# Performance work log

Measured on AMD Instinct MI355X. Metric: run time of the kernel, lower is better.

The kernel has to match this reference:

```python
import jax, jax.numpy as jnp
import numpy as np

B, TQ, TK, D, H = 2, 2048, 2048, 1024, 16
HD = D // H
MLP = 4 * D
EPS = 1e-5


def _ln(x, g, b):
    m = jnp.mean(x, axis=-1, keepdims=True)
    v = jnp.mean(jnp.square(x - m), axis=-1, keepdims=True)
    return (x - m) * jax.lax.rsqrt(v + EPS) * g + b


def setup_inputs() -> dict:
    key = jax.random.key(0)
    ks = jax.random.split(key, 16)
    s = 0.02
    inp = {
        "x": jax.random.normal(ks[0], (B, TQ, D), jnp.float32),
        "enc_out": jax.random.normal(ks[1], (B, TK, D), jnp.float32),
        "causal_mask": jnp.tril(jnp.ones((TQ, TQ), jnp.int32)),
        # LayerNorm params
        "ln1_g": jnp.ones((D,), jnp.float32), "ln1_b": jnp.zeros((D,), jnp.float32),
        "ln2_g": jnp.ones((D,), jnp.float32), "ln2_b": jnp.zeros((D,), jnp.float32),
        "ln3_g": jnp.ones((D,), jnp.float32), "ln3_b": jnp.zeros((D,), jnp.float32),
        # self-attn (weights stored [in, out])
        "qkv_w": jax.random.normal(ks[2], (D, 3 * D), jnp.float32) * s,
        "qkv_b": jnp.zeros((3 * D,), jnp.float32),
        "proj_w": jax.random.normal(ks[3], (D, D), jnp.float32) * s,
        "proj_b": jnp.zeros((D,), jnp.float32),
        # cross-attn
        "q_w": jax.random.normal(ks[4], (D, D), jnp.float32) * s,
        "q_b": jnp.zeros((D,), jnp.float32),
        "kv_w": jax.random.normal(ks[5], (D, 2 * D), jnp.float32) * s,
        "kv_b": jnp.zeros((2 * D,), jnp.float32),
        "co_w": jax.random.normal(ks[6], (D, D), jnp.float32) * s,
        "co_b": jnp.zeros((D,), jnp.float32),
        # MLP
        "mlp1_w": jax.random.normal(ks[7], (D, MLP), jnp.float32) * s,
        "mlp1_b": jnp.zeros((MLP,), jnp.float32),
        "mlp2_w": jax.random.normal(ks[8], (MLP, D), jnp.float32) * s,
        "mlp2_b": jnp.zeros((D,), jnp.float32),
    }
    return inp


def _self_attn(x, mask, qkv_w, qkv_b, proj_w, proj_b):
    b, t, d = x.shape
    qkv = (x @ qkv_w + qkv_b).reshape(b, t, 3, H, HD)
    q, k, v = qkv[:, :, 0], qkv[:, :, 1], qkv[:, :, 2]  # [b,t,H,HD]
    scale = HD ** (-0.5)
    attn = jnp.einsum('bqhd,bkhd->bhqk', q, k) * scale
    attn = jnp.where(mask[None, None] == 0, -jnp.inf, attn)
    attn = jax.nn.softmax(attn, axis=-1)
    out = jnp.einsum('bhqk,bkhd->bqhd', attn, v).reshape(b, t, d)
    return out @ proj_w + proj_b


def _cross_attn(q_in, kv_in, q_w, q_b, kv_w, kv_b, co_w, co_b):
    b, tq, d = q_in.shape
    tk = kv_in.shape[1]
    Q = (q_in @ q_w + q_b).reshape(b, tq, H, HD)
    KV = (kv_in @ kv_w + kv_b).reshape(b, tk, 2, H, HD)
    K, V = KV[:, :, 0], KV[:, :, 1]
    scale = HD ** (-0.5)
    attn = jnp.einsum('bqhd,bkhd->bhqk', Q, K) * scale
    attn = jax.nn.softmax(attn, axis=-1)
    out = jnp.einsum('bhqk,bkhd->bqhd', attn, V).reshape(b, tq, d)
    return out @ co_w + co_b


def reference(x, enc_out, causal_mask, ln1_g, ln1_b, ln2_g, ln2_b, ln3_g, ln3_b,
              qkv_w, qkv_b, proj_w, proj_b, q_w, q_b, kv_w, kv_b, co_w, co_b,
              mlp1_w, mlp1_b, mlp2_w, mlp2_b):
    x = x + _self_attn(_ln(x, ln1_g, ln1_b), causal_mask, qkv_w, qkv_b, proj_w, proj_b)
    x = x + _cross_attn(_ln(x, ln2_g, ln2_b), enc_out, q_w, q_b, kv_w, kv_b, co_w, co_b)
    h = _ln(x, ln3_g, ln3_b)
    h = jax.nn.gelu(h @ mlp1_w + mlp1_b, approximate=False) @ mlp2_w + mlp2_b
    return x + h
```

## Files before the change

### kernel.cpp

```cpp
#include <hip/hip_runtime.h>
#include <hip/hip_bf16.h>
#include <cstdint>
#include <cstddef>


#define DEV __device__ __forceinline__

typedef short bf16x8 __attribute__((ext_vector_type(8)));
typedef float f32x4  __attribute__((ext_vector_type(4)));

#define QSCALE 0.18033688011112042f

DEV unsigned short f2bf(float f) {
  unsigned int u = __builtin_bit_cast(unsigned int, f);
  u = u + 0x7FFFu + ((u >> 16) & 1u);
  return (unsigned short)(u >> 16);
}

DEV unsigned int cvt_pk_bf16(float lo, float hi) {
  unsigned int r;
  asm volatile("v_cvt_pk_bf16_f32 %0, %1, %2" : "=v"(r) : "v"(lo), "v"(hi));
  return r;
}

DEV void gload_lds16(const void* g, void* lds) {
  __builtin_amdgcn_global_load_lds(
      (const __attribute__((address_space(1))) void*)g,
      (__attribute__((address_space(3))) void*)lds, 16, 0, 0);
}

__global__ __launch_bounds__(256) void k_transpose_bf16(
    const float* __restrict__ in, unsigned short* __restrict__ out, int K, int N,
    int s0, int s1, float sc) {
  __shared__ float tile[32][33];
  const int n0 = blockIdx.x * 32, k0 = blockIdx.y * 32;
  const int tx = threadIdx.x, ty = threadIdx.y;
#pragma unroll
  for (int i = 0; i < 32; i += 8)
    tile[ty + i][tx] = in[(size_t)(k0 + ty + i) * N + n0 + tx];
  __syncthreads();
#pragma unroll
  for (int i = 0; i < 32; i += 8) {
    const int n = n0 + ty + i;
    float v = tile[tx][ty + i];
    if (n >= s0 && n < s1) v *= sc;
    out[(size_t)n * K + k0 + tx] = f2bf(v);
  }
}

__global__ __launch_bounds__(256) void k_scale_bias(
    const float* __restrict__ in, float* __restrict__ out, int n, int s0, int s1, float sc) {
  const int i = blockIdx.x * 256 + threadIdx.x;
  if (i < n) out[i] = in[i] * ((i >= s0 && i < s1) ? sc : 1.0f);
}

__global__ __launch_bounds__(256) void k_vtrans(
    const unsigned short* __restrict__ V, int ldv, int vo0,
    unsigned short* __restrict__ vt, int TK) {
  __shared__ unsigned short tile[32][33];
  const int k0 = blockIdx.x * 32;
  const int d0 = (blockIdx.y & 1) * 32;
  const int bh = blockIdx.z;
  const int b = bh >> 4, h = bh & 15;
  const int tx = threadIdx.x, ty = threadIdx.y;
  const size_t tok0 = (size_t)b * 2048;
#pragma unroll
  for (int i = 0; i < 32; i += 8)
    tile[ty + i][tx] = V[(tok0 + k0 + ty + i) * ldv + vo0 + h * 64 + d0 + tx];
  __syncthreads();
#pragma unroll
  for (int i = 0; i < 32; i += 8)
    vt[((size_t)bh * 64 + d0 + ty + i) * TK + k0 + tx] = tile[tx][ty + i];
}

__global__ __launch_bounds__(256) void k_f32_to_bf16(
    const float* __restrict__ in, unsigned short* __restrict__ out, int n4) {
  const int i = blockIdx.x * 256 + threadIdx.x;
  if (i < n4) {
    const float4 v = ((const float4*)in)[i];
    ushort4 o;
    o.x = f2bf(v.x); o.y = f2bf(v.y); o.z = f2bf(v.z); o.w = f2bf(v.w);
    ((ushort4*)out)[i] = o;
  }
}

__global__ __launch_bounds__(256) void k_ln(
    const float* __restrict__ x, const float* __restrict__ g,
    const float* __restrict__ bt, unsigned short* __restrict__ y) {
  const int row = blockIdx.x, t = threadIdx.x;
  const float4 v = ((const float4*)(x + (size_t)row * 1024))[t];
  float s1 = v.x + v.y + v.z + v.w;
  float s2 = v.x * v.x + v.y * v.y + v.z * v.z + v.w * v.w;
#pragma unroll
  for (int off = 1; off < 64; off <<= 1) {
    s1 += __shfl_xor(s1, off);
    s2 += __shfl_xor(s2, off);
  }
  __shared__ float r1[4], r2[4];
  if ((t & 63) == 0) { r1[t >> 6] = s1; r2[t >> 6] = s2; }
  __syncthreads();
  const float tot1 = r1[0] + r1[1] + r1[2] + r1[3];
  const float tot2 = r2[0] + r2[1] + r2[2] + r2[3];
  const float mean = tot1 * (1.0f / 1024.0f);
  const float var  = tot2 * (1.0f / 1024.0f) - mean * mean;
  const float rstd = rsqrtf(var + 1e-5f);
  const float4 gg = ((const float4*)g)[t];
  const float4 bb = ((const float4*)bt)[t];
  ushort4 o;
  o.x = f2bf((v.x - mean) * rstd * gg.x + bb.x);
  o.y = f2bf((v.y - mean) * rstd * gg.y + bb.y);
  o.z = f2bf((v.z - mean) * rstd * gg.z + bb.z);
  o.w = f2bf((v.w - mean) * rstd * gg.w + bb.w);
  ((ushort4*)(y + (size_t)row * 1024))[t] = o;
}

template <int EPI, int BN>
__global__ __launch_bounds__(256) void k_gemm(
    const unsigned short* __restrict__ A, const unsigned short* __restrict__ Bt,
    const float* __restrict__ bias, const float* __restrict__ resid,
    unsigned short* __restrict__ Obf, float* __restrict__ Of, int N, int K) {
  constexpr int NFR = BN / 32;
  __shared__ __align__(16) unsigned short As[128 * 32];
  __shared__ __align__(16) unsigned short Bs[BN * 32];
  const int tid = threadIdx.x;
  const int wave = tid >> 6, lane = tid & 63;
  const int nwg = gridDim.x * gridDim.y;
  const int wg = blockIdx.y * gridDim.x + blockIdx.x;
  const int swz = (wg & 7) * (nwg >> 3) + (wg >> 3);
  const int bn = swz % gridDim.x, bm = swz / gridDim.x;
  const int la = lane & 15, ks = (lane >> 4) * 8;
  const int wr = wave >> 1, wc = wave & 1;
  f32x4 acc[4][NFR] = {};
  const int rsub = lane >> 2;
  const int kk = (lane & 3) * 8;
  const unsigned short* ga = A  + (size_t)(bm * 128 + wave * 32 + rsub) * K + kk;
  const unsigned short* gb = Bt + (size_t)(bn * BN + wave * (BN / 4) + rsub) * K + kk;
  unsigned short* lA0 = &As[(wave * 32) * 32];
  unsigned short* lA1 = &As[(wave * 32 + 16) * 32];
  unsigned short* lB0 = &Bs[(wave * (BN / 4)) * 32];
  unsigned short* lB1 = &Bs[(wave * (BN / 4) + 16) * 32];
  for (int kt = 0; kt < K; kt += 32) {
    gload_lds16(ga + kt,                  lA0);
    gload_lds16(ga + kt + (size_t)16 * K, lA1);
    gload_lds16(gb + kt,                  lB0);
    if constexpr (BN == 128) gload_lds16(gb + kt + (size_t)16 * K, lB1);
    __syncthreads();
    bf16x8 af[4], bfr[NFR];
#pragma unroll
    for (int m = 0; m < 4; ++m)
      af[m] = *(const bf16x8*)&As[(wr * 64 + m * 16 + la) * 32 + ks];
#pragma unroll
    for (int n = 0; n < NFR; ++n)
      bfr[n] = *(const bf16x8*)&Bs[(wc * (BN / 2) + n * 16 + la) * 32 + ks];
#pragma unroll
    for (int m = 0; m < 4; ++m)
#pragma unroll
      for (int n = 0; n < NFR; ++n)
        acc[m][n] = __builtin_amdgcn_mfma_f32_16x16x32_bf16(af[m], bfr[n], acc[m][n], 0, 0, 0);
    __syncthreads();
  }
#pragma unroll
  for (int m = 0; m < 4; ++m) {
    const int row = bm * 128 + wr * 64 + m * 16 + (lane >> 4) * 4;
#pragma unroll
    for (int n = 0; n < NFR; ++n) {
      const int col = bn * BN + wc * (BN / 2) + n * 16 + la;
      const float bv = bias[col];
#pragma unroll
      for (int r = 0; r < 4; ++r) {
        float v = acc[m][n][r] + bv;
        const size_t idx = (size_t)(row + r) * N + col;
        if constexpr (EPI == 0) {
          Obf[idx] = f2bf(v);
        } else if constexpr (EPI == 1) {
          Of[idx] = v + resid[idx];
        } else {
          v = 0.5f * v * (1.0f + erff(v * 0.70710678118654752f));
          Obf[idx] = f2bf(v);
        }
      }
    }
  }
}

template <bool CAUSAL>
__global__ __launch_bounds__(256) void k_attn4(
    const unsigned short* __restrict__ Qb, int ldq, int qo0,
    const unsigned short* __restrict__ Kb, int ldk, int ko0,
    const unsigned short* __restrict__ Vtg,
    unsigned short* __restrict__ O, int TK) {
  __shared__ __align__(16) unsigned short Ks[2][64 * 64];
  __shared__ __align__(16) unsigned short Vs[2][64 * 64];
  __shared__ __align__(16) unsigned short Pl[4][16 * 64];
  const int qt = (blockIdx.x + blockIdx.y) & 31;
  const int h = blockIdx.y, b = blockIdx.z;
  const int bh = b * 16 + h;
  const int tid = threadIdx.x, wave = tid >> 6, lane = tid & 63;
  const int la = lane & 15, g = lane >> 4;
  const int qoff = qo0 + h * 64, koff = ko0 + h * 64;
  const size_t tok0 = (size_t)b * 2048;

  bf16x8 qf[2];
  {
    const unsigned short* qp =
        Qb + (tok0 + qt * 64 + wave * 16 + la) * ldq + qoff + g * 8;
    qf[0] = *(const bf16x8*)qp;
    qf[1] = *(const bf16x8*)(qp + 32);
  }
  f32x4 oacc[4] = {};
  float m_r = -1e30f, l_r = 0.0f;

  const int nkt = CAUSAL ? (qt + 1) : (TK >> 6);

  const int rr = lane >> 3, cc = lane & 7;
  const int sc = (cc ^ rr) * 8;
  const unsigned short* Vrow = Vtg + (size_t)bh * 64 * TK;
  auto stage = [&](int kt, int buf) {
#pragma unroll
    for (int r = 0; r < 2; ++r) {
      const int row = wave * 8 + r * 32 + rr;
      gload_lds16(Kb + (tok0 + kt * 64 + row) * ldk + koff + sc,
                  &Ks[buf][(wave * 8 + r * 32) * 64]);
      gload_lds16(Vrow + (size_t)row * TK + kt * 64 + sc,
                  &Vs[buf][(wave * 8 + r * 32) * 64]);
    }
  };

  stage(0, 0);
  int cur = 0;
  char* pw = (char*)Pl[wave];
  const int lsw = (la & 7) << 4;

  for (int kt = 0; kt < nkt; ++kt) {
    if (kt + 1 < nkt) {
      stage(kt + 1, cur ^ 1);
      asm volatile("s_waitcnt vmcnt(4)" ::: "memory");
    } else {
      asm volatile("s_waitcnt vmcnt(0)" ::: "memory");
    }
    __builtin_amdgcn_s_barrier();

    f32x4 s[4] = {};
    __builtin_amdgcn_s_setprio(1);
#pragma unroll
    for (int kc = 0; kc < 2; ++kc)
#pragma unroll
      for (int n = 0; n < 4; ++n) {
        const int key = n * 16 + la;
        const bf16x8 kfr = *(const bf16x8*)((const char*)&Ks[cur][0] +
            key * 128 + ((kc * 64 + g * 16) ^ ((key & 7) << 4)));
        s[n] = __builtin_amdgcn_mfma_f32_16x16x32_bf16(kfr, qf[kc], s[n], 0, 0, 0);
      }
    __builtin_amdgcn_s_setprio(0);

    if (CAUSAL && kt == nkt - 1) {
      const int qloc = wave * 16 + la;
#pragma unroll
      for (int n = 0; n < 4; ++n)
#pragma unroll
        for (int r = 0; r < 4; ++r)
          if (n * 16 + g * 4 + r > qloc) s[n][r] = -1e30f;
    }
    float t0 = fmaxf(fmaxf(s[0][0], s[0][1]), fmaxf(s[0][2], s[0][3]));
    float t1 = fmaxf(fmaxf(s[1][0], s[1][1]), fmaxf(s[1][2], s[1][3]));
    float t2 = fmaxf(fmaxf(s[2][0], s[2][1]), fmaxf(s[2][2], s[2][3]));
    float t3 = fmaxf(fmaxf(s[3][0], s[3][1]), fmaxf(s[3][2], s[3][3]));
    float tm = fmaxf(fmaxf(t0, t1), fmaxf(t2, t3));
    tm = fmaxf(tm, __shfl_xor(tm, 16, 64));
    tm = fmaxf(tm, __shfl_xor(tm, 32, 64));
    if (!__all(tm <= m_r + 8.0f)) {
      const float mn = fmaxf(m_r, tm);
      const float al = exp2f(m_r - mn);
      m_r = mn;
      l_r *= al;
#pragma unroll
      for (int n4 = 0; n4 < 4; ++n4)
#pragma unroll
        for (int r = 0; r < 4; ++r) oacc[n4][r] *= al;
    }
    float p[4][4];
#pragma unroll
    for (int n = 0; n < 4; ++n)
#pragma unroll
      for (int r = 0; r < 4; ++r) p[n][r] = exp2f(s[n][r] - m_r);
    float rs = ((p[0][0] + p[0][1]) + (p[0][2] + p[0][3]))
             + ((p[1][0] + p[1][1]) + (p[1][2] + p[1][3]))
             + ((p[2][0] + p[2][1]) + (p[2][2] + p[2][3]))
             + ((p[3][0] + p[3][1]) + (p[3][2] + p[3][3]));
    rs += __shfl_xor(rs, 16, 64);
    rs += __shfl_xor(rs, 32, 64);
    l_r += rs;

#pragma unroll
    for (int n = 0; n < 4; ++n)
#pragma unroll
      for (int rp = 0; rp < 2; ++rp) {
        const unsigned int w = cvt_pk_bf16(p[n][2 * rp], p[n][2 * rp + 1]);
        *(unsigned int*)(pw + la * 128 + ((n * 32 + g * 8 + rp * 4) ^ lsw)) = w;
      }
    asm volatile("s_waitcnt lgkmcnt(0)" ::: "memory");
    bf16x8 pb[2];
    pb[0] = *(const bf16x8*)(pw + la * 128 + ((0 * 64 + g * 16) ^ lsw));
    pb[1] = *(const bf16x8*)(pw + la * 128 + ((1 * 64 + g * 16) ^ lsw));

    __builtin_amdgcn_s_setprio(1);
#pragma unroll
    for (int kc = 0; kc < 2; ++kc)
#pragma unroll
      for (int n4 = 0; n4 < 4; ++n4) {
        const int d = n4 * 16 + la;
        const bf16x8 vb = *(const bf16x8*)((const char*)&Vs[cur][0] +
            d * 128 + ((kc * 64 + g * 16) ^ ((d & 7) << 4)));
        oacc[n4] = __builtin_amdgcn_mfma_f32_16x16x32_bf16(vb, pb[kc], oacc[n4], 0, 0, 0);
      }
    __builtin_amdgcn_s_setprio(0);
    asm volatile("s_waitcnt lgkmcnt(0)" ::: "memory");
    __builtin_amdgcn_s_barrier();
    cur ^= 1;
  }

  const float inv = 1.0f / l_r;
#pragma unroll
  for (int n4 = 0; n4 < 4; ++n4)
#pragma unroll
    for (int rp = 0; rp < 2; ++rp) {
      const unsigned int w = cvt_pk_bf16(oacc[n4][2 * rp] * inv, oacc[n4][2 * rp + 1] * inv);
      *(unsigned int*)(pw + la * 128 + ((n4 * 32 + g * 8 + rp * 4) ^ lsw)) = w;
    }
  asm volatile("s_waitcnt lgkmcnt(0)" ::: "memory");
  const int q2 = lane >> 2, c4 = lane & 3;
  const size_t orow = tok0 + qt * 64 + wave * 16 + q2;
#pragma unroll
  for (int h8 = 0; h8 < 2; ++h8) {
    const bf16x8 v = *(const bf16x8*)(pw + q2 * 128 +
        ((c4 * 32 + h8 * 16) ^ ((q2 & 7) << 4)));
    *(bf16x8*)&O[orow * 1024 + h * 64 + c4 * 16 + h8 * 8] = v;
  }
}

constexpr size_t SZ_1K1K  = 1024ull * 1024 * 2;
constexpr size_t OFF_WQKV = 0;                         constexpr size_t SZ_WQKV = 3072ull * 1024 * 2;
constexpr size_t OFF_WPRJ = OFF_WQKV + SZ_WQKV;
constexpr size_t OFF_WQ   = OFF_WPRJ + SZ_1K1K;
constexpr size_t OFF_WKV  = OFF_WQ + SZ_1K1K;          constexpr size_t SZ_WKV = 2048ull * 1024 * 2;
constexpr size_t OFF_WCO  = OFF_WKV + SZ_WKV;
constexpr size_t OFF_WM1  = OFF_WCO + SZ_1K1K;         constexpr size_t SZ_WM1 = 4096ull * 1024 * 2;
constexpr size_t OFF_WM2  = OFF_WM1 + SZ_WM1;          constexpr size_t SZ_WM2 = 1024ull * 4096 * 2;
constexpr size_t OFF_ENCB = OFF_WM2 + SZ_WM2;          constexpr size_t SZ_ACT = 4096ull * 1024 * 2;
constexpr size_t OFF_XCUR = OFF_ENCB + SZ_ACT;         constexpr size_t SZ_XF  = 4096ull * 1024 * 4;
constexpr size_t OFF_LNO  = OFF_XCUR + SZ_XF;
constexpr size_t OFF_BIG  = OFF_LNO + SZ_ACT;          constexpr size_t SZ_BIG = 4096ull * 4096 * 2;
constexpr size_t OFF_ATTN = OFF_BIG + SZ_BIG;
constexpr size_t OFF_QPRJ = OFF_ATTN + SZ_ACT;
constexpr size_t OFF_BQKV = OFF_QPRJ + SZ_ACT;
constexpr size_t OFF_BQ   = OFF_BQKV + 3072 * 4;
constexpr size_t WS_NEED  = OFF_BQ + 1024 * 4;

extern "C" void kernel_launch(void* const* d_in, const int* in_sizes, int n_in,
                              void* d_out, int out_size, void* d_ws, size_t ws_size,
                              hipStream_t stream) {
  (void)in_sizes; (void)n_in; (void)out_size;
  if (ws_size < WS_NEED) return;

  const float* x     = (const float*)d_in[0];
  const float* enc   = (const float*)d_in[1];
  const float* ln1g  = (const float*)d_in[3];
  const float* ln1b  = (const float*)d_in[4];
  const float* ln2g  = (const float*)d_in[5];
  const float* ln2b  = (const float*)d_in[6];
  const float* ln3g  = (const float*)d_in[7];
  const float* ln3b  = (const float*)d_in[8];
  const float* qkv_w = (const float*)d_in[9];
  const float* qkv_b = (const float*)d_in[10];
  const float* prj_w = (const float*)d_in[11];
  const float* prj_b = (const float*)d_in[12];
  const float* q_w   = (const float*)d_in[13];
  const float* q_b   = (const float*)d_in[14];
  const float* kv_w  = (const float*)d_in[15];
  const float* kv_b  = (const float*)d_in[16];
  const float* co_w  = (const float*)d_in[17];
  const float* co_b  = (const float*)d_in[18];
  const float* m1_w  = (const float*)d_in[19];
  const float* m1_b  = (const float*)d_in[20];
  const float* m2_w  = (const float*)d_in[21];
  const float* m2_b  = (const float*)d_in[22];
  float* out = (float*)d_out;

  char* ws = (char*)d_ws;
  unsigned short* wqkv = (unsigned short*)(ws + OFF_WQKV);
  unsigned short* wprj = (unsigned short*)(ws + OFF_WPRJ);
  unsigned short* wq   = (unsigned short*)(ws + OFF_WQ);
  unsigned short* wkv  = (unsigned short*)(ws + OFF_WKV);
  unsigned short* wco  = (unsigned short*)(ws + OFF_WCO);
  unsigned short* wm1  = (unsigned short*)(ws + OFF_WM1);
  unsigned short* wm2  = (unsigned short*)(ws + OFF_WM2);
  unsigned short* encb = (unsigned short*)(ws + OFF_ENCB);
  float*          xcur = (float*)(ws + OFF_XCUR);
  unsigned short* lno  = (unsigned short*)(ws + OFF_LNO);
  unsigned short* big  = (unsigned short*)(ws + OFF_BIG);
  unsigned short* attnb= (unsigned short*)(ws + OFF_ATTN);
  unsigned short* qprj = (unsigned short*)(ws + OFF_QPRJ);
  float*          bqkv = (float*)(ws + OFF_BQKV);
  float*          bq   = (float*)(ws + OFF_BQ);
  unsigned short* vtS  = big + (size_t)4096 * 3072;
  unsigned short* vtC  = big + (size_t)4096 * 2048;

  const dim3 tb(32, 8);
  k_transpose_bf16<<<dim3(3072/32, 1024/32), tb, 0, stream>>>(qkv_w, wqkv, 1024, 3072, 0, 1024, QSCALE);
  k_transpose_bf16<<<dim3(1024/32, 1024/32), tb, 0, stream>>>(prj_w, wprj, 1024, 1024, 0, 0, 1.0f);
  k_transpose_bf16<<<dim3(1024/32, 1024/32), tb, 0, stream>>>(q_w,   wq,   1024, 1024, 0, 1024, QSCALE);
  k_transpose_bf16<<<dim3(2048/32, 1024/32), tb, 0, stream>>>(kv_w,  wkv,  1024, 2048, 0, 0, 1.0f);
  k_transpose_bf16<<<dim3(1024/32, 1024/32), tb, 0, stream>>>(co_w,  wco,  1024, 1024, 0, 0, 1.0f);
  k_transpose_bf16<<<dim3(4096/32, 1024/32), tb, 0, stream>>>(m1_w,  wm1,  1024, 4096, 0, 0, 1.0f);
  k_transpose_bf16<<<dim3(1024/32, 4096/32), tb, 0, stream>>>(m2_w,  wm2,  4096, 1024, 0, 0, 1.0f);
  k_scale_bias<<<12, 256, 0, stream>>>(qkv_b, bqkv, 3072, 0, 1024, QSCALE);
  k_scale_bias<<<4, 256, 0, stream>>>(q_b, bq, 1024, 0, 1024, QSCALE);
  k_f32_to_bf16<<<4096, 256, 0, stream>>>(enc, encb, 1048576);

  k_ln<<<4096, 256, 0, stream>>>(x, ln1g, ln1b, lno);
  k_gemm<0,128><<<dim3(24, 32), 256, 0, stream>>>(lno, wqkv, bqkv, nullptr, big, nullptr, 3072, 1024);
  k_vtrans<<<dim3(64, 2, 32), tb, 0, stream>>>(big, 3072, 2048, vtS, 2048);
  k_attn4<true><<<dim3(32, 16, 2), 256, 0, stream>>>(big, 3072, 0,
                                                     big, 3072, 1024,
                                                     vtS, attnb, 2048);
  k_gemm<1,64><<<dim3(16, 32), 256, 0, stream>>>(attnb, wprj, prj_b, x, nullptr, xcur, 1024, 1024);

  k_ln<<<4096, 256, 0, stream>>>(xcur, ln2g, ln2b, lno);
  k_gemm<0,64><<<dim3(16, 32), 256, 0, stream>>>(lno,  wq,  bq,   nullptr, qprj, nullptr, 1024, 1024);
  k_gemm<0,128><<<dim3(16, 32), 256, 0, stream>>>(encb, wkv, kv_b, nullptr, big,  nullptr, 2048, 1024);
  k_vtrans<<<dim3(64, 2, 32), tb, 0, stream>>>(big, 2048, 1024, vtC, 2048);
  k_attn4<false><<<dim3(32, 16, 2), 256, 0, stream>>>(qprj, 1024, 0,
                                                      big,  2048, 0,
                                                      vtC, attnb, 2048);
  k_gemm<1,64><<<dim3(16, 32), 256, 0, stream>>>(attnb, wco, co_b, xcur, nullptr, xcur, 1024, 1024);

  k_ln<<<4096, 256, 0, stream>>>(xcur, ln3g, ln3b, lno);
  k_gemm<2,128><<<dim3(32, 32), 256, 0, stream>>>(lno, wm1, m1_b, nullptr, big, nullptr, 4096, 1024);
  k_gemm<1,64><<<dim3(16, 32), 256, 0, stream>>>(big, wm2, m2_b, xcur, nullptr, out, 1024, 4096);
}
```

Before: 651.0 us.

## Software-pipeline attention: overlap QK^T of next tile with softmax/PV of previous

Restructures the flash-attention loop so each iteration computes S for tile t while doing softmax and PV for tile t-1, letting MFMA work overlap with exp/shuffle work. V gets a triple-buffered LDS ring and K stays double-buffered. Loads are now issued right after a single barrier with a full vmcnt(0) wait. This adds LDS and register pressure (an extra score tile is kept live), and the removed trailing barrier could introduce a buffer reuse hazard.

```diff
diff --git a/kernel.cpp b/kernel.cpp
--- a/kernel.cpp
+++ b/kernel.cpp
@@ -184,13 +184,13 @@
 }
 
 template <bool CAUSAL>
-__global__ __launch_bounds__(256) void k_attn4(
+__global__ __launch_bounds__(256) void k_attn5(
     const unsigned short* __restrict__ Qb, int ldq, int qo0,
     const unsigned short* __restrict__ Kb, int ldk, int ko0,
     const unsigned short* __restrict__ Vtg,
     unsigned short* __restrict__ O, int TK) {
   __shared__ __align__(16) unsigned short Ks[2][64 * 64];
-  __shared__ __align__(16) unsigned short Vs[2][64 * 64];
+  __shared__ __align__(16) unsigned short Vs[3][64 * 64];
   __shared__ __align__(16) unsigned short Pl[4][16 * 64];
   const int qt = (blockIdx.x + blockIdx.y) & 31;
   const int h = blockIdx.y, b = blockIdx.z;
@@ -208,63 +208,40 @@
     qf[1] = *(const bf16x8*)(qp + 32);
   }
   f32x4 oacc[4] = {};
+  f32x4 sp[4];
   float m_r = -1e30f, l_r = 0.0f;
-
   const int nkt = CAUSAL ? (qt + 1) : (TK >> 6);
 
   const int rr = lane >> 3, cc = lane & 7;
   const int sc = (cc ^ rr) * 8;
   const unsigned short* Vrow = Vtg + (size_t)bh * 64 * TK;
-  auto stage = [&](int kt, int buf) {
+  auto stage = [&](int kt, unsigned short* kb, unsigned short* vb) {
 #pragma unroll
     for (int r = 0; r < 2; ++r) {
       const int row = wave * 8 + r * 32 + rr;
       gload_lds16(Kb + (tok0 + kt * 64 + row) * ldk + koff + sc,
-                  &Ks[buf][(wave * 8 + r * 32) * 64]);
+                  kb + (wave * 8 + r * 32) * 64);
       gload_lds16(Vrow + (size_t)row * TK + kt * 64 + sc,
-                  &Vs[buf][(wave * 8 + r * 32) * 64]);
+                  vb + (wave * 8 + r * 32) * 64);
     }
   };
 
-  stage(0, 0);
-  int cur = 0;
   char* pw = (char*)Pl[wave];
   const int lsw = (la & 7) << 4;
 
-  for (int kt = 0; kt < nkt; ++kt) {
-    if (kt + 1 < nkt) {
-      stage(kt + 1, cur ^ 1);
-      asm volatile("s_waitcnt vmcnt(4)" ::: "memory");
-    } else {
-      asm volatile("s_waitcnt vmcnt(0)" ::: "memory");
+  auto sm_pv = [&](const char* vbB, bool domask) {
+    if (CAUSAL && domask) {
+      const int qloc = wave * 16 + la;
+#pragma unroll
+      for (int n = 0; n < 4; ++n)
+#pragma unroll
+        for (int r = 0; r < 4; ++r)
+          if (n * 16 + g * 4 + r > qloc) sp[n][r] = -1e30f;
     }
-    __builtin_amdgcn_s_barrier();
-
-    f32x4 s[4] = {};
-    __builtin_amdgcn_s_setprio(1);
-#pragma unroll
-    for (int kc = 0; kc < 2; ++kc)
-#pragma unroll
-      for (int n = 0; n < 4; ++n) {
-        const int key = n * 16 + la;
-        const bf16x8 kfr = *(const bf16x8*)((const char*)&Ks[cur][0] +
-            key * 128 + ((kc * 64 + g * 16) ^ ((key & 7) << 4)));
-        s[n] = __builtin_amdgcn_mfma_f32_16x16x32_bf16(kfr, qf[kc], s[n], 0, 0, 0);
-      }
-    __builtin_amdgcn_s_setprio(0);
-
-    if (CAUSAL && kt == nkt - 1) {
-      const int qloc = wave * 16 + la;
-#pragma unroll
-      for (int n = 0; n < 4; ++n)
-#pragma unroll
-        for (int r = 0; r < 4; ++r)
-          if (n * 16 + g * 4 + r > qloc) s[n][r] = -1e30f;
-    }
-    float t0 = fmaxf(fmaxf(s[0][0], s[0][1]), fmaxf(s[0][2], s[0][3]));
-    float t1 = fmaxf(fmaxf(s[1][0], s[1][1]), fmaxf(s[1][2], s[1][3]));
-    float t2 = fmaxf(fmaxf(s[2][0], s[2][1]), fmaxf(s[2][2], s[2][3]));
-    float t3 = fmaxf(fmaxf(s[3][0], s[3][1]), fmaxf(s[3][2], s[3][3]));
+    float t0 = fmaxf(fmaxf(sp[0][0], sp[0][1]), fmaxf(sp[0][2], sp[0][3]));
+    float t1 = fmaxf(fmaxf(sp[1][0], sp[1][1]), fmaxf(sp[1][2], sp[1][3]));
+    float t2 = fmaxf(fmaxf(sp[2][0], sp[2][1]), fmaxf(sp[2][2], sp[2][3]));
+    float t3 = fmaxf(fmaxf(sp[3][0], sp[3][1]), fmaxf(sp[3][2], sp[3][3]));
     float tm = fmaxf(fmaxf(t0, t1), fmaxf(t2, t3));
     tm = fmaxf(tm, __shfl_xor(tm, 16, 64));
     tm = fmaxf(tm, __shfl_xor(tm, 32, 64));
@@ -282,7 +259,7 @@
 #pragma unroll
     for (int n = 0; n < 4; ++n)
 #pragma unroll
-      for (int r = 0; r < 4; ++r) p[n][r] = exp2f(s[n][r] - m_r);
+      for (int r = 0; r < 4; ++r) p[n][r] = exp2f(sp[n][r] - m_r);
     float rs = ((p[0][0] + p[0][1]) + (p[0][2] + p[0][3]))
              + ((p[1][0] + p[1][1]) + (p[1][2] + p[1][3]))
              + ((p[2][0] + p[2][1]) + (p[2][2] + p[2][3]))
@@ -290,7 +267,6 @@
     rs += __shfl_xor(rs, 16, 64);
     rs += __shfl_xor(rs, 32, 64);
     l_r += rs;
-
 #pragma unroll
     for (int n = 0; n < 4; ++n)
 #pragma unroll
@@ -299,26 +275,55 @@
         *(unsigned int*)(pw + la * 128 + ((n * 32 + g * 8 + rp * 4) ^ lsw)) = w;
       }
     asm volatile("s_waitcnt lgkmcnt(0)" ::: "memory");
-    bf16x8 pb[2];
-    pb[0] = *(const bf16x8*)(pw + la * 128 + ((0 * 64 + g * 16) ^ lsw));
-    pb[1] = *(const bf16x8*)(pw + la * 128 + ((1 * 64 + g * 16) ^ lsw));
-
+    const bf16x8 pb0 = *(const bf16x8*)(pw + la * 128 + ((g * 16) ^ lsw));
+    const bf16x8 pb1 = *(const bf16x8*)(pw + la * 128 + ((64 + g * 16) ^ lsw));
     __builtin_amdgcn_s_setprio(1);
 #pragma unroll
     for (int kc = 0; kc < 2; ++kc)
 #pragma unroll
       for (int n4 = 0; n4 < 4; ++n4) {
         const int d = n4 * 16 + la;
-        const bf16x8 vb = *(const bf16x8*)((const char*)&Vs[cur][0] +
+        const bf16x8 vfrag = *(const bf16x8*)(vbB +
             d * 128 + ((kc * 64 + g * 16) ^ ((d & 7) << 4)));
-        oacc[n4] = __builtin_amdgcn_mfma_f32_16x16x32_bf16(vb, pb[kc], oacc[n4], 0, 0, 0);
+        oacc[n4] = __builtin_amdgcn_mfma_f32_16x16x32_bf16(
+            vfrag, kc ? pb1 : pb0, oacc[n4], 0, 0, 0);
       }
     __builtin_amdgcn_s_setprio(0);
-    asm volatile("s_waitcnt lgkmcnt(0)" ::: "memory");
+  };
+
+  unsigned short* vbP = Vs[2];
+  unsigned short* vbC = Vs[0];
+  unsigned short* vbN = Vs[1];
+  stage(0, Ks[0], vbC);
+  int kcur = 0;
+
+  for (int t = 0; t < nkt; ++t) {
+    asm volatile("s_waitcnt vmcnt(0)" ::: "memory");
     __builtin_amdgcn_s_barrier();
-    cur ^= 1;
-  }
-
+    if (t + 1 < nkt) stage(t + 1, Ks[kcur ^ 1], vbN);
+
+    f32x4 sn[4] = {};
+    __builtin_amdgcn_s_setprio(1);
+#pragma unroll
+    for (int kc = 0; kc < 2; ++kc)
+#pragma unroll
+      for (int n = 0; n < 4; ++n) {
+        const int key = n * 16 + la;
+        const bf16x8 kfr = *(const bf16x8*)((const char*)Ks[kcur] +
+            key * 128 + ((kc * 64 + g * 16) ^ ((key & 7) << 4)));
+        sn[n] = __builtin_amdgcn_mfma_f32_16x16x32_bf16(kfr, qf[kc], sn[n], 0, 0, 0);
+      }
+    __builtin_amdgcn_s_setprio(0);
+
+    if (t > 0) sm_pv((const char*)vbP, false);
+
+    sp[0] = sn[0]; sp[1] = sn[1]; sp[2] = sn[2]; sp[3] = sn[3];
+    unsigned short* tmp = vbP; vbP = vbC; vbC = vbN; vbN = tmp;
+    kcur ^= 1;
+  }
+  sm_pv((const char*)vbP, true);
+
+  asm volatile("s_waitcnt lgkmcnt(0)" ::: "memory");
   const float inv = 1.0f / l_r;
 #pragma unroll
   for (int n4 = 0; n4 < 4; ++n4)
@@ -420,7 +425,7 @@
   k_ln<<<4096, 256, 0, stream>>>(x, ln1g, ln1b, lno);
   k_gemm<0,128><<<dim3(24, 32), 256, 0, stream>>>(lno, wqkv, bqkv, nullptr, big, nullptr, 3072, 1024);
   k_vtrans<<<dim3(64, 2, 32), tb, 0, stream>>>(big, 3072, 2048, vtS, 2048);
-  k_attn4<true><<<dim3(32, 16, 2), 256, 0, stream>>>(big, 3072, 0,
+  k_attn5<true><<<dim3(32, 16, 2), 256, 0, stream>>>(big, 3072, 0,
                                                      big, 3072, 1024,
                                                      vtS, attnb, 2048);
   k_gemm<1,64><<<dim3(16, 32), 256, 0, stream>>>(attnb, wprj, prj_b, x, nullptr, xcur, 1024, 1024);
@@ -429,7 +434,7 @@
   k_gemm<0,64><<<dim3(16, 32), 256, 0, stream>>>(lno,  wq,  bq,   nullptr, qprj, nullptr, 1024, 1024);
   k_gemm<0,128><<<dim3(16, 32), 256, 0, stream>>>(encb, wkv, kv_b, nullptr, big,  nullptr, 2048, 1024);
   k_vtrans<<<dim3(64, 2, 32), tb, 0, stream>>>(big, 2048, 1024, vtC, 2048);
-  k_attn4<false><<<dim3(32, 16, 2), 256, 0, stream>>>(qprj, 1024, 0,
+  k_attn5<false><<<dim3(32, 16, 2), 256, 0, stream>>>(qprj, 1024, 0,
                                                       big,  2048, 0,
                                                       vtC, attnb, 2048);
   k_gemm<1,64><<<dim3(16, 32), 256, 0, stream>>>(attnb, wco, co_b, xcur, nullptr, xcur, 1024, 1024);
```

Measured after the change: 672.1 us. +3.2%, slower.

## Double GEMM K-tile to 64 with XOR-swizzled LDS layout

Applied to the files above, without the earlier changes.

Raises the GEMM K-step from 32 to 64 per barrier pair, so each iteration does two MFMA sub-steps and the number of __syncthreads drops by half. Loads are reorganised so each 8-lane group fetches one 128-byte row, with the column chunk XOR-swizzled by row, and fragment reads apply the same swizzle to avoid LDS bank conflicts. This doubles LDS usage per block, which may lower occupancy, and there is still no double buffering of loads against compute.

```diff
diff --git a/kernel.cpp b/kernel.cpp
--- a/kernel.cpp
+++ b/kernel.cpp
@@ -120,43 +120,50 @@
     const float* __restrict__ bias, const float* __restrict__ resid,
     unsigned short* __restrict__ Obf, float* __restrict__ Of, int N, int K) {
   constexpr int NFR = BN / 32;
-  __shared__ __align__(16) unsigned short As[128 * 32];
-  __shared__ __align__(16) unsigned short Bs[BN * 32];
+  __shared__ __align__(16) unsigned short As[128 * 64];
+  __shared__ __align__(16) unsigned short Bs[BN * 64];
   const int tid = threadIdx.x;
   const int wave = tid >> 6, lane = tid & 63;
   const int nwg = gridDim.x * gridDim.y;
   const int wg = blockIdx.y * gridDim.x + blockIdx.x;
   const int swz = (wg & 7) * (nwg >> 3) + (wg >> 3);
   const int bn = swz % gridDim.x, bm = swz / gridDim.x;
-  const int la = lane & 15, ks = (lane >> 4) * 8;
+  const int la = lane & 15, g = lane >> 4;
   const int wr = wave >> 1, wc = wave & 1;
   f32x4 acc[4][NFR] = {};
-  const int rsub = lane >> 2;
-  const int kk = (lane & 3) * 8;
-  const unsigned short* ga = A  + (size_t)(bm * 128 + wave * 32 + rsub) * K + kk;
-  const unsigned short* gb = Bt + (size_t)(bn * BN + wave * (BN / 4) + rsub) * K + kk;
-  unsigned short* lA0 = &As[(wave * 32) * 32];
-  unsigned short* lA1 = &As[(wave * 32 + 16) * 32];
-  unsigned short* lB0 = &Bs[(wave * (BN / 4)) * 32];
-  unsigned short* lB1 = &Bs[(wave * (BN / 4) + 16) * 32];
-  for (int kt = 0; kt < K; kt += 32) {
-    gload_lds16(ga + kt,                  lA0);
-    gload_lds16(ga + kt + (size_t)16 * K, lA1);
-    gload_lds16(gb + kt,                  lB0);
-    if constexpr (BN == 128) gload_lds16(gb + kt + (size_t)16 * K, lB1);
+  const int rrow = lane >> 3;
+  const int sc = ((lane & 7) ^ rrow) * 8;
+  const unsigned short* ga = A  + (size_t)(bm * 128 + wave * 8 + rrow) * K + sc;
+  const unsigned short* gb = Bt + (size_t)(bn * BN  + wave * 8 + rrow) * K + sc;
+  for (int kt = 0; kt < K; kt += 64) {
+#pragma unroll
+    for (int r = 0; r < 4; ++r)
+      gload_lds16(ga + (size_t)(r * 32) * K + kt, &As[(r * 32 + wave * 8) * 64]);
+#pragma unroll
+    for (int r = 0; r < BN / 32; ++r)
+      gload_lds16(gb + (size_t)(r * 32) * K + kt, &Bs[(r * 32 + wave * 8) * 64]);
     __syncthreads();
-    bf16x8 af[4], bfr[NFR];
-#pragma unroll
-    for (int m = 0; m < 4; ++m)
-      af[m] = *(const bf16x8*)&As[(wr * 64 + m * 16 + la) * 32 + ks];
-#pragma unroll
-    for (int n = 0; n < NFR; ++n)
-      bfr[n] = *(const bf16x8*)&Bs[(wc * (BN / 2) + n * 16 + la) * 32 + ks];
-#pragma unroll
-    for (int m = 0; m < 4; ++m)
-#pragma unroll
-      for (int n = 0; n < NFR; ++n)
-        acc[m][n] = __builtin_amdgcn_mfma_f32_16x16x32_bf16(af[m], bfr[n], acc[m][n], 0, 0, 0);
+#pragma unroll
+    for (int kc = 0; kc < 2; ++kc) {
+      bf16x8 af[4], bfr[NFR];
+#pragma unroll
+      for (int m = 0; m < 4; ++m) {
+        const int row = wr * 64 + m * 16 + la;
+        af[m] = *(const bf16x8*)((const char*)As + row * 128 +
+                                 ((kc * 64 + g * 16) ^ ((row & 7) << 4)));
+      }
+#pragma unroll
+      for (int n = 0; n < NFR; ++n) {
+        const int row = wc * (BN / 2) + n * 16 + la;
+        bfr[n] = *(const bf16x8*)((const char*)Bs + row * 128 +
+                                  ((kc * 64 + g * 16) ^ ((row & 7) << 4)));
+      }
+#pragma unroll
+      for (int m = 0; m < 4; ++m)
+#pragma unroll
+        for (int n = 0; n < NFR; ++n)
+          acc[m][n] = __builtin_amdgcn_mfma_f32_16x16x32_bf16(af[m], bfr[n], acc[m][n], 0, 0, 0);
+    }
     __syncthreads();
   }
 #pragma unroll
```

Measured after the change: 626.9 us. 1.04x faster.
